# Performance work log

Hardware: AMD Instinct MI355X
Metric: run time of the kernel (lower is better)

The kernel has to match this reference:

```python
import jax, jax.numpy as jnp
from jax import lax
import numpy as np

V = 50000   # location_size
H = 512     # hidden_size (embedding width == LSTM width in original code)
B = 128     # number of ragged sequences (batch)
L = 512     # max sequence length (padded)


def setup_inputs() -> dict:
    key = jax.random.key(0)
    ks = jax.random.split(key, 8)
    tokens = jax.random.randint(ks[0], (B, L), 0, V)           # assembled ragged token ids, padded
    lengths = jax.random.randint(ks[1], (B,), 1, L + 1)        # valid length per sequence (>=1)
    s = 1.0 / np.sqrt(H)
    emb = jax.random.normal(ks[2], (V, H), jnp.float32)
    W_ih = jax.random.uniform(ks[3], (4 * H, H), jnp.float32, -s, s)
    W_hh = jax.random.uniform(ks[4], (4 * H, H), jnp.float32, -s, s)
    b_ih = jax.random.uniform(ks[5], (4 * H,), jnp.float32, -s, s)
    b_hh = jax.random.uniform(ks[6], (4 * H,), jnp.float32, -s, s)
    W_fc = jax.random.uniform(ks[7], (V, H), jnp.float32, -s, s)
    b_fc = jnp.zeros((V,), jnp.float32)
    return {"tokens": tokens, "lengths": lengths, "emb": emb,
            "W_ih": W_ih, "W_hh": W_hh, "b_ih": b_ih, "b_hh": b_hh,
            "W_fc": W_fc, "b_fc": b_fc}


def reference(tokens, lengths, emb, W_ih, W_hh, b_ih, b_hh, W_fc, b_fc):
    # Embedding gather (the ragged per-trajectory slice+concat collapses to this gather)
    x = emb[tokens]                                             # [B, L, H]
    # Precompute input contribution to gates once: [B, L, 4H]
    x_proj = jnp.einsum('blh,gh->blg', x, W_ih) + b_ih + b_hh
    h0 = jnp.zeros((B, H), x.dtype)
    c0 = jnp.zeros((B, H), x.dtype)

    def step(carry, inp):
        h, c = carry
        xp, t = inp                                             # xp: [B, 4H]
        gates = xp + h @ W_hh.T
        i, f, g, o = jnp.split(gates, 4, axis=-1)               # PyTorch gate order i,f,g,o
        i = jax.nn.sigmoid(i)
        f = jax.nn.sigmoid(f)
        g = jnp.tanh(g)
        o = jax.nn.sigmoid(o)
        c_new = f * c + i * g
        h_new = o * jnp.tanh(c_new)
        valid = (t < lengths)[:, None]                          # freeze state past each length
        return (jnp.where(valid, h_new, h), jnp.where(valid, c_new, c)), None

    (hT, _), _ = lax.scan(step, (h0, c0),
                          (jnp.swapaxes(x_proj, 0, 1), jnp.arange(L)))
    # fc on final hidden state of (single) last layer, squeeze(0) of [1,B,H] -> [B,H]
    return hT @ W_fc.T + b_fc                                    # [B, V]
```

## Files before the change

### kernel.cpp

```cpp
#include <hip/hip_runtime.h>
#include <stdint.h>


#define NB   128
#define LMAX 512
#define HD   512
#define G4   2048
#define NV   50000

#define H0C_OFF     0
#define T0_OFF      131072
#define T1_OFF      393216
#define C_OFF       655360
#define EMB16_OFF   917504
#define EMB16_BYTES (NV * HD * 2)
#define WIH16_OFF   (EMB16_OFF + EMB16_BYTES)
#define WIH16_BYTES (G4 * HD * 2)
#define XP_OFF      (WIH16_OFF + WIH16_BYTES)
#define INIT_W4     57344

typedef _Float16 f16;
typedef _Float16 half8  __attribute__((ext_vector_type(8)));
typedef float    float4v __attribute__((ext_vector_type(4)));
typedef uint32_t u32;
typedef unsigned long long u64;
typedef uint32_t u32x4 __attribute__((ext_vector_type(4)));

__device__ __forceinline__ half8 cvt8(const float* p) {
  float4v a = *(const float4v*)p;
  float4v b = *(const float4v*)(p + 4);
  half8 r;
  r[0] = (f16)a[0]; r[1] = (f16)a[1]; r[2] = (f16)a[2]; r[3] = (f16)a[3];
  r[4] = (f16)b[0]; r[5] = (f16)b[1]; r[6] = (f16)b[2]; r[7] = (f16)b[3];
  return r;
}
__device__ __forceinline__ float sigmoidf_(float x) { return 1.0f / (1.0f + __expf(-x)); }
__device__ __forceinline__ float tanhf_(float x)    { return 1.0f - 2.0f / (1.0f + __expf(2.0f * x)); }

__device__ __forceinline__ void barx() {
  __builtin_amdgcn_sched_barrier(0);
  __builtin_amdgcn_s_waitcnt(0xC07F);
  __builtin_amdgcn_s_barrier();
  __builtin_amdgcn_sched_barrier(0);
}

extern "C" __global__ void k0_init(u32x4* ws4) {
  int idx = blockIdx.x * 256 + threadIdx.x;
  u32x4 z = {0u, 0u, 0u, 0u};
  if (idx < INIT_W4) ws4[idx] = z;
}

extern "C" __global__ void __launch_bounds__(256)
k_cvt(const float* __restrict__ src, f16* __restrict__ dst, int n8) {
  int i = blockIdx.x * 256 + threadIdx.x;
  if (i >= n8) return;
  ((half8*)dst)[i] = cvt8(src + (size_t)i * 8);
}

extern "C" __global__ void __launch_bounds__(256)
k1_xproj(const int* __restrict__ tokens, const int* __restrict__ lengths,
         const f16* __restrict__ emb16, const f16* __restrict__ wih16,
         const float* __restrict__ bih, const float* __restrict__ bhh,
         f16* __restrict__ xp, int t0c, int TC) {
  int b  = blockIdx.x;
  int mt = blockIdx.y;
  int nt = blockIdx.z;
  int len = lengths[b];
  int t0 = t0c + mt * 64;
  if (t0 >= len) return;

  __shared__ f16 As[64 * 512];
  int tid = threadIdx.x;

  #pragma unroll
  for (int it = 0; it < 16; ++it) {
    int gl = tid + 256 * it;
    int row = gl >> 6, gi = gl & 63;
    int tok = tokens[b * LMAX + t0 + row];
    half8 v = *(const half8*)(emb16 + (size_t)tok * HD + gi * 8);
    *(half8*)&As[row * 512 + ((gi ^ (row & 7)) * 8)] = v;
  }
  __syncthreads();

  int wave = tid >> 6, lane = tid & 63;
  int quad = lane >> 4, l15 = lane & 15;
  int col0 = nt * 128 + wave * 32;

  float4v acc[4][2] = {};
  for (int c = 0; c < 16; ++c) {
    half8 b0 = *(const half8*)(wih16 + (size_t)(col0 + l15) * HD + c * 32 + quad * 8);
    half8 b1 = *(const half8*)(wih16 + (size_t)(col0 + 16 + l15) * HD + c * 32 + quad * 8);
    #pragma unroll
    for (int mm = 0; mm < 4; ++mm) {
      int row = mm * 16 + l15;
      half8 a = *(const half8*)&As[row * 512 + (((c * 4 + quad) ^ (row & 7)) * 8)];
      acc[mm][0] = __builtin_amdgcn_mfma_f32_16x16x32_f16(a, b0, acc[mm][0], 0, 0, 0);
      acc[mm][1] = __builtin_amdgcn_mfma_f32_16x16x32_f16(a, b1, acc[mm][1], 0, 0, 0);
    }
  }

  #pragma unroll
  for (int q = 0; q < 2; ++q) {
    int gcol = col0 + q * 16 + l15;
    float bias = bih[gcol] + bhh[gcol];
    #pragma unroll
    for (int mm = 0; mm < 4; ++mm) {
      #pragma unroll
      for (int j = 0; j < 4; ++j) {
        int t = t0 + mm * 16 + quad * 4 + j;
        if (t < len)
          xp[((size_t)b * TC + (t - t0c)) * G4 + gcol] = (f16)(acc[mm][q][j] + bias);
      }
    }
  }
}

extern "C" __global__ void __launch_bounds__(256, 1)
k2_lstm(const int* __restrict__ lengths, const float* __restrict__ Whh,
        const f16* __restrict__ xp, u64* __restrict__ tb0, u64* __restrict__ tb1,
        f16* __restrict__ h0c, float* __restrict__ cbuf, int t0c, int TC) {
  int wg = blockIdx.x;
  int pair = wg & 3, memb = wg >> 2;
  int grpA = pair * 2, grpB = grpA + 1;
  int s0A = grpA * 16, s0B = grpB * 16;
  int tid = threadIdx.x;

  int gmA = 0, gmB = 0;
  for (int i = 0; i < 16; ++i) { int l = lengths[s0A + i]; gmA = l > gmA ? l : gmA; }
  for (int i = 0; i < 16; ++i) { int l = lengths[s0B + i]; gmB = l > gmB ? l : gmB; }
  int tendA = (t0c + TC < gmA) ? (t0c + TC) : gmA;
  int tendB = (t0c + TC < gmB) ? (t0c + TC) : gmB;
  int tmax = tendA > tendB ? tendA : tendB;
  if (t0c >= tmax) return;

  __shared__ f16 HsA[16 * 512], HsB[16 * 512];
  __shared__ float gA[16][133], gB[16][133];

  int wave = tid >> 6, lane = tid & 63;
  int quad = lane >> 4, l15 = lane & 15;

  half8 wf0[16], wf1[16];
  {
    const float* r0 = Whh + (size_t)(wave * 512 + memb * 32 + l15) * HD;
    const float* r1 = r0 + (size_t)16 * HD;
    #pragma unroll
    for (int c = 0; c < 16; ++c) {
      wf0[c] = cvt8(r0 + c * 32 + quad * 8);
      wf1[c] = cvt8(r1 + c * 32 + quad * 8);
    }
  }

  int sE = tid >> 4, kE = tid & 15, kk0 = kE * 2;
  int lenA = lengths[s0A + sE], lenB = lengths[s0B + sE];
  float cA0 = cbuf[(size_t)(s0A + sE) * HD + memb * 32 + kk0];
  float cA1 = cbuf[(size_t)(s0A + sE) * HD + memb * 32 + kk0 + 1];
  float cB0 = cbuf[(size_t)(s0B + sE) * HD + memb * 32 + kk0];
  float cB1 = cbuf[(size_t)(s0B + sE) * HD + memb * 32 + kk0 + 1];

  size_t wA = (size_t)(s0A + sE) * 256 + memb * 16 + kE;
  size_t wB = (size_t)(s0B + sE) * 256 + memb * 16 + kE;
  const u64* hin0 = (t0c & 1) ? tb1 : tb0;
  u32 hpA = (u32)hin0[wA];
  u32 hpB = (u32)hin0[wB];

  int gG = tid >> 2, w4 = (tid & 3) * 2;

  u64 a[16], b[16];
  if (t0c < tendA) {
    #pragma unroll
    for (int r = 0; r < 16; ++r)
      a[r] = __hip_atomic_load(hin0 + (size_t)(s0A + r) * 256 + tid,
                               __ATOMIC_RELAXED, __HIP_MEMORY_SCOPE_AGENT);
  }

  for (int t = t0c; t < tmax; ++t) {
    bool actA = t < tendA, actB = t < tendB;
    const u64* tin = (t & 1) ? tb1 : tb0;
    u64*       tout = (t & 1) ? tb0 : tb1;
    u32 tg = (u32)t;

    u32 xA[4], xB[4];
    if (actA) {
      const f16* p = xp + ((size_t)(s0A + sE) * TC + (t - t0c)) * G4 + memb * 32 + kk0;
      xA[0] = *(const u32*)p;          xA[1] = *(const u32*)(p + 512);
      xA[2] = *(const u32*)(p + 1024); xA[3] = *(const u32*)(p + 1536);
    }
    if (actB) {
      const f16* p = xp + ((size_t)(s0B + sE) * TC + (t - t0c)) * G4 + memb * 32 + kk0;
      xB[0] = *(const u32*)p;          xB[1] = *(const u32*)(p + 512);
      xB[2] = *(const u32*)(p + 1024); xB[3] = *(const u32*)(p + 1536);
    }

    if (actA) {
      for (;;) {
        u32 bad = 0;
        #pragma unroll
        for (int r = 0; r < 16; ++r)
          bad |= ((u32)(a[r] >> 32) != tg) ? (1u << r) : 0u;
        if (!bad) break;
        __builtin_amdgcn_s_sleep(1);
        #pragma unroll
        for (int r = 0; r < 16; ++r)
          if (bad & (1u << r))
            a[r] = __hip_atomic_load(tin + (size_t)(s0A + r) * 256 + tid,
                                     __ATOMIC_RELAXED, __HIP_MEMORY_SCOPE_AGENT);
      }
      #pragma unroll
      for (int r = 0; r < 16; ++r)
        *(u32*)&HsA[r * 512 + ((gG ^ (r & 7)) << 3) + w4] = (u32)a[r];
      barx();
    }

    if (actB) {
      #pragma unroll
      for (int r = 0; r < 16; ++r)
        b[r] = __hip_atomic_load(tin + (size_t)(s0B + r) * 256 + tid,
                                 __ATOMIC_RELAXED, __HIP_MEMORY_SCOPE_AGENT);
    }

    if (actA) {
      float4v a0e = {}, a0o = {}, a1e = {}, a1o = {};
      #pragma unroll
      for (int c = 0; c < 16; ++c) {
        half8 av = *(const half8*)&HsA[l15 * 512 + (((c * 4 + quad) ^ (l15 & 7)) * 8)];
        if (c & 1) {
          a0o = __builtin_amdgcn_mfma_f32_16x16x32_f16(av, wf0[c], a0o, 0, 0, 0);
          a1o = __builtin_amdgcn_mfma_f32_16x16x32_f16(av, wf1[c], a1o, 0, 0, 0);
        } else {
          a0e = __builtin_amdgcn_mfma_f32_16x16x32_f16(av, wf0[c], a0e, 0, 0, 0);
          a1e = __builtin_amdgcn_mfma_f32_16x16x32_f16(av, wf1[c], a1e, 0, 0, 0);
        }
      }
      float4v g0 = a0e + a0o, g1 = a1e + a1o;
      #pragma unroll
      for (int j = 0; j < 4; ++j) {
        gA[quad * 4 + j][wave * 32 + l15]      = g0[j];
        gA[quad * 4 + j][wave * 32 + 16 + l15] = g1[j];
      }
      barx();
      if (t < lenA) {
        union { u32 u; f16 h[2]; } xi, xf, xg, xo, hp;
        xi.u = xA[0]; xf.u = xA[1]; xg.u = xA[2]; xo.u = xA[3];
        float i0 = sigmoidf_(gA[sE][kk0]          + (float)xi.h[0]);
        float i1 = sigmoidf_(gA[sE][kk0 + 1]      + (float)xi.h[1]);
        float f0 = sigmoidf_(gA[sE][32 + kk0]     + (float)xf.h[0]);
        float f1 = sigmoidf_(gA[sE][32 + kk0 + 1] + (float)xf.h[1]);
        float q0 = tanhf_  (gA[sE][64 + kk0]      + (float)xg.h[0]);
        float q1 = tanhf_  (gA[sE][64 + kk0 + 1]  + (float)xg.h[1]);
        float o0 = sigmoidf_(gA[sE][96 + kk0]     + (float)xo.h[0]);
        float o1 = sigmoidf_(gA[sE][96 + kk0 + 1] + (float)xo.h[1]);
        cA0 = f0 * cA0 + i0 * q0;
        cA1 = f1 * cA1 + i1 * q1;
        hp.h[0] = (f16)(o0 * tanhf_(cA0));
        hp.h[1] = (f16)(o1 * tanhf_(cA1));
        hpA = hp.u;
      }
      u64 wv = ((u64)(u32)(t + 1) << 32) | (u64)hpA;
      __hip_atomic_store(tout + wA, wv, __ATOMIC_RELAXED, __HIP_MEMORY_SCOPE_AGENT);
    }

    if (actB) {
      for (;;) {
        u32 bad = 0;
        #pragma unroll
        for (int r = 0; r < 16; ++r)
          bad |= ((u32)(b[r] >> 32) != tg) ? (1u << r) : 0u;
        if (!bad) break;
        __builtin_amdgcn_s_sleep(1);
        #pragma unroll
        for (int r = 0; r < 16; ++r)
          if (bad & (1u << r))
            b[r] = __hip_atomic_load(tin + (size_t)(s0B + r) * 256 + tid,
                                     __ATOMIC_RELAXED, __HIP_MEMORY_SCOPE_AGENT);
      }
      #pragma unroll
      for (int r = 0; r < 16; ++r)
        *(u32*)&HsB[r * 512 + ((gG ^ (r & 7)) << 3) + w4] = (u32)b[r];
      if (t + 1 < tendA) {
        #pragma unroll
        for (int r = 0; r < 16; ++r)
          a[r] = __hip_atomic_load(tout + (size_t)(s0A + r) * 256 + tid,
                                   __ATOMIC_RELAXED, __HIP_MEMORY_SCOPE_AGENT);
      }
      barx();
      float4v a0e = {}, a0o = {}, a1e = {}, a1o = {};
      #pragma unroll
      for (int c = 0; c < 16; ++c) {
        half8 av = *(const half8*)&HsB[l15 * 512 + (((c * 4 + quad) ^ (l15 & 7)) * 8)];
        if (c & 1) {
          a0o = __builtin_amdgcn_mfma_f32_16x16x32_f16(av, wf0[c], a0o, 0, 0, 0);
          a1o = __builtin_amdgcn_mfma_f32_16x16x32_f16(av, wf1[c], a1o, 0, 0, 0);
        } else {
          a0e = __builtin_amdgcn_mfma_f32_16x16x32_f16(av, wf0[c], a0e, 0, 0, 0);
          a1e = __builtin_amdgcn_mfma_f32_16x16x32_f16(av, wf1[c], a1e, 0, 0, 0);
        }
      }
      float4v g0 = a0e + a0o, g1 = a1e + a1o;
      #pragma unroll
      for (int j = 0; j < 4; ++j) {
        gB[quad * 4 + j][wave * 32 + l15]      = g0[j];
        gB[quad * 4 + j][wave * 32 + 16 + l15] = g1[j];
      }
      barx();
      if (t < lenB) {
        union { u32 u; f16 h[2]; } xi, xf, xg, xo, hp;
        xi.u = xB[0]; xf.u = xB[1]; xg.u = xB[2]; xo.u = xB[3];
        float i0 = sigmoidf_(gB[sE][kk0]          + (float)xi.h[0]);
        float i1 = sigmoidf_(gB[sE][kk0 + 1]      + (float)xi.h[1]);
        float f0 = sigmoidf_(gB[sE][32 + kk0]     + (float)xf.h[0]);
        float f1 = sigmoidf_(gB[sE][32 + kk0 + 1] + (float)xf.h[1]);
        float q0 = tanhf_  (gB[sE][64 + kk0]      + (float)xg.h[0]);
        float q1 = tanhf_  (gB[sE][64 + kk0 + 1]  + (float)xg.h[1]);
        float o0 = sigmoidf_(gB[sE][96 + kk0]     + (float)xo.h[0]);
        float o1 = sigmoidf_(gB[sE][96 + kk0 + 1] + (float)xo.h[1]);
        cB0 = f0 * cB0 + i0 * q0;
        cB1 = f1 * cB1 + i1 * q1;
        hp.h[0] = (f16)(o0 * tanhf_(cB0));
        hp.h[1] = (f16)(o1 * tanhf_(cB1));
        hpB = hp.u;
      }
      u64 wv = ((u64)(u32)(t + 1) << 32) | (u64)hpB;
      __hip_atomic_store(tout + wB, wv, __ATOMIC_RELAXED, __HIP_MEMORY_SCOPE_AGENT);
    } else if (t + 1 < tendA) {
      #pragma unroll
      for (int r = 0; r < 16; ++r)
        a[r] = __hip_atomic_load(tout + (size_t)(s0A + r) * 256 + tid,
                                 __ATOMIC_RELAXED, __HIP_MEMORY_SCOPE_AGENT);
    }
  }

  cbuf[(size_t)(s0A + sE) * HD + memb * 32 + kk0]     = cA0;
  cbuf[(size_t)(s0A + sE) * HD + memb * 32 + kk0 + 1] = cA1;
  cbuf[(size_t)(s0B + sE) * HD + memb * 32 + kk0]     = cB0;
  cbuf[(size_t)(s0B + sE) * HD + memb * 32 + kk0 + 1] = cB1;

  *(u32*)&h0c[(size_t)(s0A + sE) * HD + memb * 32 + kk0] = hpA;
  *(u32*)&h0c[(size_t)(s0B + sE) * HD + memb * 32 + kk0] = hpB;
}

extern "C" __global__ void __launch_bounds__(256)
k3_fc(const f16* __restrict__ hT, const float* __restrict__ Wfc,
      const float* __restrict__ bfc, float* __restrict__ out) {
  int tid = threadIdx.x;
  int wave = tid >> 6, lane = tid & 63, quad = lane >> 4, l15 = lane & 15;
  int v = blockIdx.x * 64 + wave * 16 + l15;
  int vc = v < NV ? v : NV - 1;
  float4v acc[8] = {};
  for (int c = 0; c < 16; ++c) {
    half8 bfr = cvt8(Wfc + (size_t)vc * HD + c * 32 + quad * 8);
    #pragma unroll
    for (int mt = 0; mt < 8; ++mt) {
      half8 afr = *(const half8*)&hT[(size_t)(mt * 16 + l15) * HD + c * 32 + quad * 8];
      acc[mt] = __builtin_amdgcn_mfma_f32_16x16x32_f16(afr, bfr, acc[mt], 0, 0, 0);
    }
  }
  if (v < NV) {
    float bias = bfc[v];
    #pragma unroll
    for (int mt = 0; mt < 8; ++mt)
      #pragma unroll
      for (int j = 0; j < 4; ++j)
        out[(size_t)(mt * 16 + quad * 4 + j) * NV + v] = acc[mt][j] + bias;
  }
}

extern "C" void kernel_launch(void* const* d_in, const int* in_sizes, int n_in,
                              void* d_out, int out_size, void* d_ws, size_t ws_size,
                              hipStream_t stream) {
  (void)in_sizes; (void)n_in; (void)out_size;
  const int*   tokens  = (const int*)d_in[0];
  const int*   lengths = (const int*)d_in[1];
  const float* emb     = (const float*)d_in[2];
  const float* Wih     = (const float*)d_in[3];
  const float* Whh     = (const float*)d_in[4];
  const float* bih     = (const float*)d_in[5];
  const float* bhh     = (const float*)d_in[6];
  const float* Wfc     = (const float*)d_in[7];
  const float* bfc     = (const float*)d_in[8];
  float* out = (float*)d_out;
  char* ws = (char*)d_ws;

  f16*  h0c  = (f16*)(ws + H0C_OFF);
  u64*  tb0  = (u64*)(ws + T0_OFF);
  u64*  tb1  = (u64*)(ws + T1_OFF);
  float* cbuf = (float*)(ws + C_OFF);
  f16* emb16 = (f16*)(ws + EMB16_OFF);
  f16* wih16 = (f16*)(ws + WIH16_OFF);
  f16* xp    = (f16*)(ws + XP_OFF);

  int TC = 512;
  while (TC > 64 && (size_t)XP_OFF + (size_t)NB * TC * G4 * 2 > ws_size) TC >>= 1;

  hipLaunchKernelGGL(k0_init, dim3(224), dim3(256), 0, stream, (u32x4*)ws);
  hipLaunchKernelGGL(k_cvt, dim3((NV * HD / 8 + 255) / 256), dim3(256), 0, stream,
                     emb, emb16, NV * HD / 8);
  hipLaunchKernelGGL(k_cvt, dim3((G4 * HD / 8 + 255) / 256), dim3(256), 0, stream,
                     Wih, wih16, G4 * HD / 8);
  for (int t0 = 0; t0 < LMAX; t0 += TC) {
    hipLaunchKernelGGL(k1_xproj, dim3(NB, TC / 64, 16), dim3(256), 0, stream,
                       tokens, lengths, emb16, wih16, bih, bhh, xp, t0, TC);
    hipLaunchKernelGGL(k2_lstm, dim3(64), dim3(256), 0, stream,
                       lengths, Whh, xp, tb0, tb1, h0c, cbuf, t0, TC);
  }
  hipLaunchKernelGGL(k3_fc, dim3((NV + 63) / 64), dim3(256), 0, stream,
                     h0c, Wfc, bfc, out);
}
```

Before: 2.614 ms.

## Give each LSTM workgroup one sequence group instead of two interleaved groups

The recurrent kernel previously had each of 64 workgroups interleave two 16-sequence groups (A and B) so that the MFMA work of one group overlapped the spin-wait of the other. Now there are 128 workgroups, each handling one group with a single loop and no interleaving. This doubles the number of CUs running the recurrence and halves the serial work per workgroup per step. In exchange it loses the latency hiding between the two groups, and the cross-workgroup sync now has to cover more participants.

Measured after the change: 2.164 ms. 17.2% less time.

```diff
diff --git a/kernel.cpp b/kernel.cpp
--- a/kernel.cpp
+++ b/kernel.cpp
@@ -120,21 +120,17 @@
         const f16* __restrict__ xp, u64* __restrict__ tb0, u64* __restrict__ tb1,
         f16* __restrict__ h0c, float* __restrict__ cbuf, int t0c, int TC) {
   int wg = blockIdx.x;
-  int pair = wg & 3, memb = wg >> 2;
-  int grpA = pair * 2, grpB = grpA + 1;
-  int s0A = grpA * 16, s0B = grpB * 16;
+  int grp = wg & 7, memb = wg >> 3;
+  int s0 = grp * 16;
   int tid = threadIdx.x;
 
-  int gmA = 0, gmB = 0;
-  for (int i = 0; i < 16; ++i) { int l = lengths[s0A + i]; gmA = l > gmA ? l : gmA; }
-  for (int i = 0; i < 16; ++i) { int l = lengths[s0B + i]; gmB = l > gmB ? l : gmB; }
-  int tendA = (t0c + TC < gmA) ? (t0c + TC) : gmA;
-  int tendB = (t0c + TC < gmB) ? (t0c + TC) : gmB;
-  int tmax = tendA > tendB ? tendA : tendB;
-  if (t0c >= tmax) return;
-
-  __shared__ f16 HsA[16 * 512], HsB[16 * 512];
-  __shared__ float gA[16][133], gB[16][133];
+  int gm = 0;
+  for (int i = 0; i < 16; ++i) { int l = lengths[s0 + i]; gm = l > gm ? l : gm; }
+  int tend = (t0c + TC < gm) ? (t0c + TC) : gm;
+  if (t0c >= tend) return;
+
+  __shared__ f16 Hs[16 * 512];
+  __shared__ float gS[16][133];
 
   int wave = tid >> 6, lane = tid & 63;
   int quad = lane >> 4, l15 = lane & 15;
@@ -151,191 +147,105 @@
   }
 
   int sE = tid >> 4, kE = tid & 15, kk0 = kE * 2;
-  int lenA = lengths[s0A + sE], lenB = lengths[s0B + sE];
-  float cA0 = cbuf[(size_t)(s0A + sE) * HD + memb * 32 + kk0];
-  float cA1 = cbuf[(size_t)(s0A + sE) * HD + memb * 32 + kk0 + 1];
-  float cB0 = cbuf[(size_t)(s0B + sE) * HD + memb * 32 + kk0];
-  float cB1 = cbuf[(size_t)(s0B + sE) * HD + memb * 32 + kk0 + 1];
-
-  size_t wA = (size_t)(s0A + sE) * 256 + memb * 16 + kE;
-  size_t wB = (size_t)(s0B + sE) * 256 + memb * 16 + kE;
+  int len = lengths[s0 + sE];
+  float c0 = cbuf[(size_t)(s0 + sE) * HD + memb * 32 + kk0];
+  float c1 = cbuf[(size_t)(s0 + sE) * HD + memb * 32 + kk0 + 1];
+
+  size_t wIdx = (size_t)(s0 + sE) * 256 + memb * 16 + kE;
   const u64* hin0 = (t0c & 1) ? tb1 : tb0;
-  u32 hpA = (u32)hin0[wA];
-  u32 hpB = (u32)hin0[wB];
+  u32 hp = (u32)hin0[wIdx];
 
   int gG = tid >> 2, w4 = (tid & 3) * 2;
 
-  u64 a[16], b[16];
-  if (t0c < tendA) {
-    #pragma unroll
-    for (int r = 0; r < 16; ++r)
-      a[r] = __hip_atomic_load(hin0 + (size_t)(s0A + r) * 256 + tid,
-                               __ATOMIC_RELAXED, __HIP_MEMORY_SCOPE_AGENT);
-  }
-
-  for (int t = t0c; t < tmax; ++t) {
-    bool actA = t < tendA, actB = t < tendB;
-    const u64* tin = (t & 1) ? tb1 : tb0;
+  u64 a[16];
+  #pragma unroll
+  for (int r = 0; r < 16; ++r)
+    a[r] = __hip_atomic_load(hin0 + (size_t)(s0 + r) * 256 + tid,
+                             __ATOMIC_RELAXED, __HIP_MEMORY_SCOPE_AGENT);
+
+  for (int t = t0c; t < tend; ++t) {
+    const u64* tin  = (t & 1) ? tb1 : tb0;
     u64*       tout = (t & 1) ? tb0 : tb1;
     u32 tg = (u32)t;
 
-    u32 xA[4], xB[4];
-    if (actA) {
-      const f16* p = xp + ((size_t)(s0A + sE) * TC + (t - t0c)) * G4 + memb * 32 + kk0;
-      xA[0] = *(const u32*)p;          xA[1] = *(const u32*)(p + 512);
-      xA[2] = *(const u32*)(p + 1024); xA[3] = *(const u32*)(p + 1536);
-    }
-    if (actB) {
-      const f16* p = xp + ((size_t)(s0B + sE) * TC + (t - t0c)) * G4 + memb * 32 + kk0;
-      xB[0] = *(const u32*)p;          xB[1] = *(const u32*)(p + 512);
-      xB[2] = *(const u32*)(p + 1024); xB[3] = *(const u32*)(p + 1536);
-    }
-
-    if (actA) {
-      for (;;) {
-        u32 bad = 0;
-        #pragma unroll
-        for (int r = 0; r < 16; ++r)
-          bad |= ((u32)(a[r] >> 32) != tg) ? (1u << r) : 0u;
-        if (!bad) break;
-        __builtin_amdgcn_s_sleep(1);
-        #pragma unroll
-        for (int r = 0; r < 16; ++r)
-          if (bad & (1u << r))
-            a[r] = __hip_atomic_load(tin + (size_t)(s0A + r) * 256 + tid,
-                                     __ATOMIC_RELAXED, __HIP_MEMORY_SCOPE_AGENT);
+    u32 x4[4];
+    {
+      const f16* p = xp + ((size_t)(s0 + sE) * TC + (t - t0c)) * G4 + memb * 32 + kk0;
+      x4[0] = *(const u32*)p;          x4[1] = *(const u32*)(p + 512);
+      x4[2] = *(const u32*)(p + 1024); x4[3] = *(const u32*)(p + 1536);
+    }
+
+    for (;;) {
+      u32 bad = 0;
+      #pragma unroll
+      for (int r = 0; r < 16; ++r)
+        bad |= ((u32)(a[r] >> 32) != tg) ? (1u << r) : 0u;
+      if (!bad) break;
+      __builtin_amdgcn_s_sleep(1);
+      #pragma unroll
+      for (int r = 0; r < 16; ++r)
+        if (bad & (1u << r))
+          a[r] = __hip_atomic_load(tin + (size_t)(s0 + r) * 256 + tid,
+                                   __ATOMIC_RELAXED, __HIP_MEMORY_SCOPE_AGENT);
+    }
+
+    #pragma unroll
+    for (int r = 0; r < 16; ++r)
+      *(u32*)&Hs[r * 512 + ((gG ^ (r & 7)) << 3) + w4] = (u32)a[r];
+    barx();
+
+    float4v a0e = {}, a0o = {}, a1e = {}, a1o = {};
+    #pragma unroll
+    for (int c = 0; c < 16; ++c) {
+      half8 av = *(const half8*)&Hs[l15 * 512 + (((c * 4 + quad) ^ (l15 & 7)) * 8)];
+      if (c & 1) {
+        a0o = __builtin_amdgcn_mfma_f32_16x16x32_f16(av, wf0[c], a0o, 0, 0, 0);
+        a1o = __builtin_amdgcn_mfma_f32_16x16x32_f16(av, wf1[c], a1o, 0, 0, 0);
+      } else {
+        a0e = __builtin_amdgcn_mfma_f32_16x16x32_f16(av, wf0[c], a0e, 0, 0, 0);
+        a1e = __builtin_amdgcn_mfma_f32_16x16x32_f16(av, wf1[c], a1e, 0, 0, 0);
       }
+    }
+    float4v g0 = a0e + a0o, g1 = a1e + a1o;
+    #pragma unroll
+    for (int j = 0; j < 4; ++j) {
+      gS[quad * 4 + j][wave * 32 + l15]      = g0[j];
+      gS[quad * 4 + j][wave * 32 + 16 + l15] = g1[j];
+    }
+    barx();
+
+    if (t < len) {
+      union { u32 u; f16 h[2]; } xi, xf, xg, xo, hpk;
+      xi.u = x4[0]; xf.u = x4[1]; xg.u = x4[2]; xo.u = x4[3];
+      float i0 = sigmoidf_(gS[sE][kk0]          + (float)xi.h[0]);
+      float i1 = sigmoidf_(gS[sE][kk0 + 1]      + (float)xi.h[1]);
+      float f0 = sigmoidf_(gS[sE][32 + kk0]     + (float)xf.h[0]);
+      float f1 = sigmoidf_(gS[sE][32 + kk0 + 1] + (float)xf.h[1]);
+      float q0 = tanhf_  (gS[sE][64 + kk0]      + (float)xg.h[0]);
+      float q1 = tanhf_  (gS[sE][64 + kk0 + 1]  + (float)xg.h[1]);
+      float o0 = sigmoidf_(gS[sE][96 + kk0]     + (float)xo.h[0]);
+      float o1 = sigmoidf_(gS[sE][96 + kk0 + 1] + (float)xo.h[1]);
+      c0 = f0 * c0 + i0 * q0;
+      c1 = f1 * c1 + i1 * q1;
+      hpk.h[0] = (f16)(o0 * tanhf_(c0));
+      hpk.h[1] = (f16)(o1 * tanhf_(c1));
+      hp = hpk.u;
+    }
+    u64 wv = ((u64)(u32)(t + 1) << 32) | (u64)hp;
+    __hip_atomic_store(tout + wIdx, wv, __ATOMIC_RELAXED, __HIP_MEMORY_SCOPE_AGENT);
+
+    if (t + 1 < tend) {
       #pragma unroll
       for (int r = 0; r < 16; ++r)
-        *(u32*)&HsA[r * 512 + ((gG ^ (r & 7)) << 3) + w4] = (u32)a[r];
-      barx();
-    }
-
-    if (actB) {
-      #pragma unroll
-      for (int r = 0; r < 16; ++r)
-        b[r] = __hip_atomic_load(tin + (size_t)(s0B + r) * 256 + tid,
+        a[r] = __hip_atomic_load(tout + (size_t)(s0 + r) * 256 + tid,
                                  __ATOMIC_RELAXED, __HIP_MEMORY_SCOPE_AGENT);
     }
-
-    if (actA) {
-      float4v a0e = {}, a0o = {}, a1e = {}, a1o = {};
-      #pragma unroll
-      for (int c = 0; c < 16; ++c) {
-        half8 av = *(const half8*)&HsA[l15 * 512 + (((c * 4 + quad) ^ (l15 & 7)) * 8)];
-        if (c & 1) {
-          a0o = __builtin_amdgcn_mfma_f32_16x16x32_f16(av, wf0[c], a0o, 0, 0, 0);
-          a1o = __builtin_amdgcn_mfma_f32_16x16x32_f16(av, wf1[c], a1o, 0, 0, 0);
-        } else {
-          a0e = __builtin_amdgcn_mfma_f32_16x16x32_f16(av, wf0[c], a0e, 0, 0, 0);
-          a1e = __builtin_amdgcn_mfma_f32_16x16x32_f16(av, wf1[c], a1e, 0, 0, 0);
-        }
-      }
-      float4v g0 = a0e + a0o, g1 = a1e + a1o;
-      #pragma unroll
-      for (int j = 0; j < 4; ++j) {
-        gA[quad * 4 + j][wave * 32 + l15]      = g0[j];
-        gA[quad * 4 + j][wave * 32 + 16 + l15] = g1[j];
-      }
-      barx();
-      if (t < lenA) {
-        union { u32 u; f16 h[2]; } xi, xf, xg, xo, hp;
-        xi.u = xA[0]; xf.u = xA[1]; xg.u = xA[2]; xo.u = xA[3];
-        float i0 = sigmoidf_(gA[sE][kk0]          + (float)xi.h[0]);
-        float i1 = sigmoidf_(gA[sE][kk0 + 1]      + (float)xi.h[1]);
-        float f0 = sigmoidf_(gA[sE][32 + kk0]     + (float)xf.h[0]);
-        float f1 = sigmoidf_(gA[sE][32 + kk0 + 1] + (float)xf.h[1]);
-        float q0 = tanhf_  (gA[sE][64 + kk0]      + (float)xg.h[0]);
-        float q1 = tanhf_  (gA[sE][64 + kk0 + 1]  + (float)xg.h[1]);
-        float o0 = sigmoidf_(gA[sE][96 + kk0]     + (float)xo.h[0]);
-        float o1 = sigmoidf_(gA[sE][96 + kk0 + 1] + (float)xo.h[1]);
-        cA0 = f0 * cA0 + i0 * q0;
-        cA1 = f1 * cA1 + i1 * q1;
-        hp.h[0] = (f16)(o0 * tanhf_(cA0));
-        hp.h[1] = (f16)(o1 * tanhf_(cA1));
-        hpA = hp.u;
-      }
-      u64 wv = ((u64)(u32)(t + 1) << 32) | (u64)hpA;
-      __hip_atomic_store(tout + wA, wv, __ATOMIC_RELAXED, __HIP_MEMORY_SCOPE_AGENT);
-    }
-
-    if (actB) {
-      for (;;) {
-        u32 bad = 0;
-        #pragma unroll
-        for (int r = 0; r < 16; ++r)
-          bad |= ((u32)(b[r] >> 32) != tg) ? (1u << r) : 0u;
-        if (!bad) break;
-        __builtin_amdgcn_s_sleep(1);
-        #pragma unroll
-        for (int r = 0; r < 16; ++r)
-          if (bad & (1u << r))
-            b[r] = __hip_atomic_load(tin + (size_t)(s0B + r) * 256 + tid,
-                                     __ATOMIC_RELAXED, __HIP_MEMORY_SCOPE_AGENT);
-      }
-      #pragma unroll
-      for (int r = 0; r < 16; ++r)
-        *(u32*)&HsB[r * 512 + ((gG ^ (r & 7)) << 3) + w4] = (u32)b[r];
-      if (t + 1 < tendA) {
-        #pragma unroll
-        for (int r = 0; r < 16; ++r)
-          a[r] = __hip_atomic_load(tout + (size_t)(s0A + r) * 256 + tid,
-                                   __ATOMIC_RELAXED, __HIP_MEMORY_SCOPE_AGENT);
-      }
-      barx();
-      float4v a0e = {}, a0o = {}, a1e = {}, a1o = {};
-      #pragma unroll
-      for (int c = 0; c < 16; ++c) {
-        half8 av = *(const half8*)&HsB[l15 * 512 + (((c * 4 + quad) ^ (l15 & 7)) * 8)];
-        if (c & 1) {
-          a0o = __builtin_amdgcn_mfma_f32_16x16x32_f16(av, wf0[c], a0o, 0, 0, 0);
-          a1o = __builtin_amdgcn_mfma_f32_16x16x32_f16(av, wf1[c], a1o, 0, 0, 0);
-        } else {
-          a0e = __builtin_amdgcn_mfma_f32_16x16x32_f16(av, wf0[c], a0e, 0, 0, 0);
-          a1e = __builtin_amdgcn_mfma_f32_16x16x32_f16(av, wf1[c], a1e, 0, 0, 0);
-        }
-      }
-      float4v g0 = a0e + a0o, g1 = a1e + a1o;
-      #pragma unroll
-      for (int j = 0; j < 4; ++j) {
-        gB[quad * 4 + j][wave * 32 + l15]      = g0[j];
-        gB[quad * 4 + j][wave * 32 + 16 + l15] = g1[j];
-      }
-      barx();
-      if (t < lenB) {
-        union { u32 u; f16 h[2]; } xi, xf, xg, xo, hp;
-        xi.u = xB[0]; xf.u = xB[1]; xg.u = xB[2]; xo.u = xB[3];
-        float i0 = sigmoidf_(gB[sE][kk0]          + (float)xi.h[0]);
-        float i1 = sigmoidf_(gB[sE][kk0 + 1]      + (float)xi.h[1]);
-        float f0 = sigmoidf_(gB[sE][32 + kk0]     + (float)xf.h[0]);
-        float f1 = sigmoidf_(gB[sE][32 + kk0 + 1] + (float)xf.h[1]);
-        float q0 = tanhf_  (gB[sE][64 + kk0]      + (float)xg.h[0]);
-        float q1 = tanhf_  (gB[sE][64 + kk0 + 1]  + (float)xg.h[1]);
-        float o0 = sigmoidf_(gB[sE][96 + kk0]     + (float)xo.h[0]);
-        float o1 = sigmoidf_(gB[sE][96 + kk0 + 1] + (float)xo.h[1]);
-        cB0 = f0 * cB0 + i0 * q0;
-        cB1 = f1 * cB1 + i1 * q1;
-        hp.h[0] = (f16)(o0 * tanhf_(cB0));
-        hp.h[1] = (f16)(o1 * tanhf_(cB1));
-        hpB = hp.u;
-      }
-      u64 wv = ((u64)(u32)(t + 1) << 32) | (u64)hpB;
-      __hip_atomic_store(tout + wB, wv, __ATOMIC_RELAXED, __HIP_MEMORY_SCOPE_AGENT);
-    } else if (t + 1 < tendA) {
-      #pragma unroll
-      for (int r = 0; r < 16; ++r)
-        a[r] = __hip_atomic_load(tout + (size_t)(s0A + r) * 256 + tid,
-                                 __ATOMIC_RELAXED, __HIP_MEMORY_SCOPE_AGENT);
-    }
-  }
-
-  cbuf[(size_t)(s0A + sE) * HD + memb * 32 + kk0]     = cA0;
-  cbuf[(size_t)(s0A + sE) * HD + memb * 32 + kk0 + 1] = cA1;
-  cbuf[(size_t)(s0B + sE) * HD + memb * 32 + kk0]     = cB0;
-  cbuf[(size_t)(s0B + sE) * HD + memb * 32 + kk0 + 1] = cB1;
-
-  *(u32*)&h0c[(size_t)(s0A + sE) * HD + memb * 32 + kk0] = hpA;
-  *(u32*)&h0c[(size_t)(s0B + sE) * HD + memb * 32 + kk0] = hpB;
+  }
+
+  cbuf[(size_t)(s0 + sE) * HD + memb * 32 + kk0]     = c0;
+  cbuf[(size_t)(s0 + sE) * HD + memb * 32 + kk0 + 1] = c1;
+
+  *(u32*)&h0c[(size_t)(s0 + sE) * HD + memb * 32 + kk0] = hp;
 }
 
 extern "C" __global__ void __launch_bounds__(256)
@@ -399,7 +309,7 @@
   for (int t0 = 0; t0 < LMAX; t0 += TC) {
     hipLaunchKernelGGL(k1_xproj, dim3(NB, TC / 64, 16), dim3(256), 0, stream,
                        tokens, lengths, emb16, wih16, bih, bhh, xp, t0, TC);
-    hipLaunchKernelGGL(k2_lstm, dim3(64), dim3(256), 0, stream,
+    hipLaunchKernelGGL(k2_lstm, dim3(128), dim3(256), 0, stream,
                        lengths, Whh, xp, tb0, tb1, h0c, cbuf, t0, TC);
   }
   hipLaunchKernelGGL(k3_fc, dim3((NV + 63) / 64), dim3(256), 0, stream,
```
